# Performance work log

Measured on AMD Instinct MI355X. Metric: run time of the kernel, lower is better.

Reference implementation:

```python
import jax, jax.numpy as jnp
import numpy as np


def setup_inputs() -> dict:
    key = jax.random.key(0)
    kx, kw = jax.random.split(key)
    x = jax.random.normal(kx, (32, 128, 64, 64), dtype=jnp.float32)
    weights = jax.random.normal(kw, (256, 128, 3, 3), dtype=jnp.float32) * 0.05
    return {"x": x, "weights": weights}


def reference(x, weights):
    # Valid-padding, stride-1, no-bias 2D cross-correlation, identical math
    # to the nested-loop HandmadeConv2d (sum over in_ch, kH, kW per output pixel).
    return jax.lax.conv_general_dilated(
        x, weights,
        window_strides=(1, 1),
        padding="VALID",
        dimension_numbers=("NCHW", "OIHW", "NCHW"),
    )
```

## Files before the change

### kernel.cpp

```cpp
#include <hip/hip_runtime.h>
#include <hip/hip_bf16.h>

typedef unsigned short ushort;
typedef unsigned int uint;
typedef __bf16 bf16x8 __attribute__((ext_vector_type(8)));
typedef float f32x4 __attribute__((ext_vector_type(4)));
typedef uint uint4v __attribute__((ext_vector_type(4)));
typedef uint uint2v __attribute__((ext_vector_type(2)));

#define CI 128
#define HIN 64
#define WIN 64
#define CO 256
#define HO 62
#define WO 62
#define NB 32
#define KTOT 1152
#define PIXIMG 3844
#define NPIX 123008
#define XIMG 524288
#define BK 64
#define NKT 18

__device__ __forceinline__ ushort f2bf(float f) {
  uint u = __builtin_bit_cast(uint, f);
  u += 0x7fffu + ((u >> 16) & 1u);
  return (ushort)(u >> 16);
}

__global__ void repack_w_kernel(const float* __restrict__ w, ushort* __restrict__ w2) {
  const int co = blockIdx.x;
  for (int idx = threadIdx.x; idx < KTOT; idx += 256) {
    const int t  = idx >> 7;
    const int ci = idx & 127;
    w2[co * KTOT + idx] = f2bf(w[(co * CI + ci) * 9 + t]);
  }
}

#define XPAD 132
__global__ __launch_bounds__(256) void repack_x_kernel(const float* __restrict__ x,
                                                       ushort* __restrict__ x2) {
  __shared__ float t[WIN * XPAD];
  const int n = blockIdx.y;
  const int h = blockIdx.x;
  const int tid = threadIdx.x;
  const float* src = x + ((size_t)n * CI * HIN + h) * WIN;
  #pragma unroll
  for (int it = 0; it < 8; ++it) {
    const int idx = it * 256 + tid;
    const int ci  = idx >> 4;
    const int w4  = (idx & 15) * 4;
    const float4 v = *reinterpret_cast<const float4*>(src + (size_t)ci * (HIN * WIN) + w4);
    t[(w4 + 0) * XPAD + ci] = v.x;
    t[(w4 + 1) * XPAD + ci] = v.y;
    t[(w4 + 2) * XPAD + ci] = v.z;
    t[(w4 + 3) * XPAD + ci] = v.w;
  }
  __syncthreads();
  ushort* dst = x2 + ((size_t)(n * HIN + h) * WIN) * CI;
  #pragma unroll
  for (int it = 0; it < 4; ++it) {
    const int idx = it * 256 + tid;
    const int w   = idx >> 4;
    const int cig = idx & 15;
    const float* p = &t[w * XPAD + cig * 8];
    uint4v q;
    q[0] = (uint)f2bf(p[0]) | ((uint)f2bf(p[1]) << 16);
    q[1] = (uint)f2bf(p[2]) | ((uint)f2bf(p[3]) << 16);
    q[2] = (uint)f2bf(p[4]) | ((uint)f2bf(p[5]) << 16);
    q[3] = (uint)f2bf(p[6]) | ((uint)f2bf(p[7]) << 16);
    *reinterpret_cast<uint4v*>(dst + (size_t)w * CI + cig * 8) = q;
  }
}

__global__ __launch_bounds__(256, 4)
void conv_nhwc_kernel(const ushort* __restrict__ x2, const ushort* __restrict__ w2,
                      float* __restrict__ out)
{
  __shared__ alignas(16) ushort a_lds[128 * 64];
  __shared__ alignas(16) ushort b_lds[128 * 64];

  const int tid  = threadIdx.x;
  const int lane = tid & 63;
  const int wid  = tid >> 6;
  const int wrow = wid >> 1;
  const int wcol = wid & 1;

  const int nwg = 1922, q8 = nwg >> 3, r8 = nwg & 7;
  const int wg  = blockIdx.x;
  const int xcd = wg & 7, sidx = wg >> 3;
  const int logical = (xcd < r8 ? xcd * (q8 + 1) : r8 * (q8 + 1) + (xcd - r8) * q8) + sidx;
  const int co0 = (logical & 1) * 128;
  const int p0  = (logical >> 1) * 128;

  const int lrow = lane >> 3;
  const int lc   = (lane & 7) ^ lrow;

  const ushort* pB[4];
  #pragma unroll
  for (int i = 0; i < 4; ++i) {
    const int row   = wid * 32 + i * 8 + lrow;
    const int pglob = p0 + row;
    const int nimg  = pglob / PIXIMG;
    const int prem  = pglob - nimg * PIXIMG;
    const int oh    = prem / WO;
    const int ow    = prem - oh * WO;
    pB[i] = x2 + (size_t)((nimg * HIN + oh) * WIN + ow) * CI + lc * 8;
  }
  const ushort* pA = w2 + (size_t)(co0 + wid * 32 + lrow) * KTOT + lc * 8;

  const int frow_a = wrow * 64 + (lane & 15);
  const int frow_b = wcol * 64 + (lane & 15);
  int aoff[2], boff[2];
  #pragma unroll
  for (int kk = 0; kk < 2; ++kk) {
    const int chk = (kk * 4 + (lane >> 4)) ^ (lane & 7);
    aoff[kk] = frow_a * 64 + chk * 8;
    boff[kk] = frow_b * 64 + chk * 8;
  }

  f32x4 acc[4][4];
  #pragma unroll
  for (int i = 0; i < 4; ++i)
    #pragma unroll
    for (int j = 0; j < 4; ++j)
      acc[i][j] = (f32x4){0.f, 0.f, 0.f, 0.f};

  #pragma unroll
  for (int kt = 0; kt < NKT; ++kt) {
    if (kt) __syncthreads();

    const int tap   = kt >> 1;
    const int rr    = (tap * 11) >> 5;
    const int ss    = tap - rr * 3;
    const int coffB = (rr * WIN + ss) * CI + (kt & 1) * 64;
    const int coffA = kt * 64;

    #pragma unroll
    for (int i = 0; i < 4; ++i) {
      const ushort* src = pA + (size_t)i * (8 * KTOT) + coffA;
      __builtin_amdgcn_global_load_lds(
          (const __attribute__((address_space(1))) uint*)(const void*)src,
          (__attribute__((address_space(3))) uint*)(void*)&a_lds[wid * 2048 + i * 512],
          16, 0, 0);
    }
    #pragma unroll
    for (int i = 0; i < 4; ++i) {
      const ushort* src = pB[i] + coffB;
      __builtin_amdgcn_global_load_lds(
          (const __attribute__((address_space(1))) uint*)(const void*)src,
          (__attribute__((address_space(3))) uint*)(void*)&b_lds[wid * 2048 + i * 512],
          16, 0, 0);
    }

    __syncthreads();

    #pragma unroll
    for (int kk = 0; kk < 2; ++kk) {
      bf16x8 af[4], bb[4];
      #pragma unroll
      for (int mi = 0; mi < 4; ++mi)
        af[mi] = *reinterpret_cast<const bf16x8*>(&a_lds[aoff[kk] + mi * (16 * 64)]);
      #pragma unroll
      for (int ni = 0; ni < 4; ++ni)
        bb[ni] = *reinterpret_cast<const bf16x8*>(&b_lds[boff[kk] + ni * (16 * 64)]);
      #pragma unroll
      for (int mi = 0; mi < 4; ++mi)
        #pragma unroll
        for (int ni = 0; ni < 4; ++ni)
          acc[mi][ni] = __builtin_amdgcn_mfma_f32_16x16x32_bf16(af[mi], bb[ni], acc[mi][ni], 0, 0, 0);
    }
  }

  #pragma unroll
  for (int ni = 0; ni < 4; ++ni) {
    const int pix = p0 + wcol * 64 + ni * 16 + (lane & 15);
    const int n2  = pix / PIXIMG;
    const int pr2 = pix - n2 * PIXIMG;
    float* ob = out + (size_t)n2 * (CO * PIXIMG) + pr2
                    + (size_t)(co0 + wrow * 64 + ((lane >> 4) * 4)) * PIXIMG;
    #pragma unroll
    for (int mi = 0; mi < 4; ++mi) {
      float* po = ob + (size_t)mi * (16 * PIXIMG);
      #pragma unroll
      for (int r = 0; r < 4; ++r)
        po[(size_t)r * PIXIMG] = acc[mi][ni][r];
    }
  }
}

__global__ __launch_bounds__(256, 3)
void conv_fallback_kernel(const float* __restrict__ x, const float* __restrict__ wt,
                          float* __restrict__ out)
{
  __shared__ alignas(16) ushort a_lds[128 * 64];
  __shared__ alignas(16) ushort b_lds[128 * 64];

  const int tid  = threadIdx.x;
  const int lane = tid & 63;
  const int wid  = tid >> 6;
  const int wrow = wid >> 1;
  const int wcol = wid & 1;
  const int co0 = blockIdx.x * 128;
  const int p0  = blockIdx.y * 128;

  const int pl    = tid & 127;
  const int kgsel = __builtin_amdgcn_readfirstlane(tid >> 7);
  const int pglob = p0 + pl;
  const int nimg  = pglob / PIXIMG;
  const int prem  = pglob - nimg * PIXIMG;
  const int oh    = prem / WO;
  const int ow    = prem - oh * WO;
  const int xpix  = nimg * XIMG + oh * WIN + ow;

  const int frow_a = wrow * 64 + (lane & 15);
  const int frow_b = wcol * 64 + (lane & 15);
  int aoff[2], boff[2];
  #pragma unroll
  for (int kk = 0; kk < 2; ++kk) {
    const int chk = (kk * 4 + (lane >> 4)) ^ (lane & 7);
    aoff[kk] = frow_a * 64 + chk * 8;
    boff[kk] = frow_b * 64 + chk * 8;
  }

  f32x4 acc[4][4];
  #pragma unroll
  for (int i = 0; i < 4; ++i)
    #pragma unroll
    for (int j = 0; j < 4; ++j)
      acc[i][j] = (f32x4){0.f, 0.f, 0.f, 0.f};

  for (int kt = 0; kt < NKT; ++kt) {
    const int k0 = kt * BK;
    if (kt) __syncthreads();

    #pragma unroll
    for (int it = 0; it < 4; ++it) {
      const int kg = kgsel + it * 2;
      uint pk[4];
      #pragma unroll
      for (int j = 0; j < 8; ++j) {
        const int k  = k0 + kg * 8 + j;
        const int ci = k / 9;
        const int rs = k - ci * 9;
        const int r  = rs / 3;
        const int s  = rs - r * 3;
        const ushort u = f2bf(x[xpix + ci * (HIN * WIN) + r * WIN + s]);
        if (j & 1) pk[j >> 1] |= ((uint)u) << 16;
        else       pk[j >> 1]  = (uint)u;
      }
      uint4v q = {pk[0], pk[1], pk[2], pk[3]};
      *reinterpret_cast<uint4v*>(&b_lds[pl * 64 + ((kg ^ (pl & 7)) * 8)]) = q;
    }

    #pragma unroll
    for (int i = 0; i < 8; ++i) {
      const int id  = i * 256 + tid;
      const int row = id >> 4;
      const int c4  = id & 15;
      const float4 v = *reinterpret_cast<const float4*>(
          wt + (size_t)(co0 + row) * KTOT + k0 + c4 * 4);
      uint2v q;
      q[0] = (uint)f2bf(v.x) | ((uint)f2bf(v.y) << 16);
      q[1] = (uint)f2bf(v.z) | ((uint)f2bf(v.w) << 16);
      *reinterpret_cast<uint2v*>(
          &a_lds[row * 64 + (((c4 >> 1) ^ (row & 7)) * 8) + (c4 & 1) * 4]) = q;
    }

    __syncthreads();

    #pragma unroll
    for (int kk = 0; kk < 2; ++kk) {
      bf16x8 af[4], bb[4];
      #pragma unroll
      for (int mi = 0; mi < 4; ++mi)
        af[mi] = *reinterpret_cast<const bf16x8*>(&a_lds[aoff[kk] + mi * (16 * 64)]);
      #pragma unroll
      for (int ni = 0; ni < 4; ++ni)
        bb[ni] = *reinterpret_cast<const bf16x8*>(&b_lds[boff[kk] + ni * (16 * 64)]);
      #pragma unroll
      for (int mi = 0; mi < 4; ++mi)
        #pragma unroll
        for (int ni = 0; ni < 4; ++ni)
          acc[mi][ni] = __builtin_amdgcn_mfma_f32_16x16x32_bf16(af[mi], bb[ni], acc[mi][ni], 0, 0, 0);
    }
  }

  #pragma unroll
  for (int ni = 0; ni < 4; ++ni) {
    const int pix = p0 + wcol * 64 + ni * 16 + (lane & 15);
    const int n2  = pix / PIXIMG;
    const int pr2 = pix - n2 * PIXIMG;
    float* ob = out + (size_t)n2 * (CO * PIXIMG) + pr2
                    + (size_t)(co0 + wrow * 64 + ((lane >> 4) * 4)) * PIXIMG;
    #pragma unroll
    for (int mi = 0; mi < 4; ++mi) {
      float* po = ob + (size_t)mi * (16 * PIXIMG);
      #pragma unroll
      for (int r = 0; r < 4; ++r)
        po[(size_t)r * PIXIMG] = acc[mi][ni][r];
    }
  }
}

extern "C" void kernel_launch(void* const* d_in, const int* in_sizes, int n_in,
                              void* d_out, int out_size, void* d_ws, size_t ws_size,
                              hipStream_t stream) {
  const float* x  = (const float*)d_in[0];
  const float* wt = (const float*)d_in[1];
  float* out = (float*)d_out;

  ushort* w2 = (ushort*)d_ws;
  ushort* x2 = (ushort*)((char*)d_ws + 589824);

  const size_t need = 589824 + (size_t)NB * XIMG * 2;

  if (ws_size >= need) {
    repack_w_kernel<<<dim3(CO), dim3(256), 0, stream>>>(wt, w2);
    repack_x_kernel<<<dim3(HIN, NB), dim3(256), 0, stream>>>(x, x2);
    conv_nhwc_kernel<<<dim3(1922), dim3(256), 0, stream>>>(x2, w2, out);
  } else {
    conv_fallback_kernel<<<dim3(CO / 128, NPIX / 128), dim3(256), 0, stream>>>(x, wt, out);
  }
}
```

Measured before the change: 104.7 us.

## Replace conv GEMM with 256x256-tile, 8-wave, double-buffered phased pipeline

Replaces the 128x128-tile, 4-wave conv kernel with a 256-pixel by 256-output-channel tile per 512-thread block. It double-buffers 128 KB of LDS and splits each k-step into four MFMA phases that interleave LDS fragment reads, global-to-LDS prefetch of the next k-tiles and barriers, with s_setprio raised around MFMA bursts. The larger tile is meant to halve global reads per FLOP and hide load latency behind compute. In exchange it drops the XCD-aware block remapping, leaves only 481 blocks (under two waves across the CUs), and clamps the out-of-range tail pixels.

Result: slower. 123.4 us (+17.8%).

```diff
diff --git a/kernel.cpp b/kernel.cpp
--- a/kernel.cpp
+++ b/kernel.cpp
@@ -19,7 +19,6 @@
 #define PIXIMG 3844
 #define NPIX 123008
 #define XIMG 524288
-#define BK 64
 #define NKT 18
 
 __device__ __forceinline__ ushort f2bf(float f) {
@@ -73,118 +72,165 @@
   }
 }
 
-__global__ __launch_bounds__(256, 4)
-void conv_nhwc_kernel(const ushort* __restrict__ x2, const ushort* __restrict__ w2,
-                      float* __restrict__ out)
+
+#define GLOAD(SRC, DSTOFF) \
+  __builtin_amdgcn_global_load_lds( \
+      (const __attribute__((address_space(1))) uint*)(const void*)(SRC), \
+      (__attribute__((address_space(3))) uint*)(void*)&lds[DSTOFF], 16, 0, 0)
+
+#define STAGE_A(DB, SLOT, KT) do { \
+  const int _ca = (KT) * 64; \
+  GLOAD(w2 + aOff[(SLOT) >> 1][0] + _ca, (DB) + (SLOT) * 8192 + stgu);       \
+  GLOAD(w2 + aOff[(SLOT) >> 1][1] + _ca, (DB) + (SLOT) * 8192 + stgu + 512); \
+} while (0)
+
+#define STAGE_B(DB, SLOT, KT) do { \
+  const int _tp = (KT) >> 1; \
+  const int _rr = (_tp * 11) >> 5; \
+  const int _cb = (_rr * WIN + (_tp - _rr * 3)) * CI + ((KT) & 1) * 64; \
+  GLOAD(x2 + bOff[(SLOT) >> 1][0] + _cb, (DB) + (SLOT) * 8192 + stgu);       \
+  GLOAD(x2 + bOff[(SLOT) >> 1][1] + _cb, (DB) + (SLOT) * 8192 + stgu + 512); \
+} while (0)
+
+#define PH_LOADS(LDB, ASLOT, BSLOT) do { \
+  _Pragma("unroll") for (int mf = 0; mf < 4; ++mf) { \
+    fa0[mf] = *reinterpret_cast<const bf16x8*>(&lds[(LDB) + (ASLOT) * 8192 + arow + mf * 1024 + ck0]); \
+    fa1[mf] = *reinterpret_cast<const bf16x8*>(&lds[(LDB) + (ASLOT) * 8192 + arow + mf * 1024 + ck1]); } \
+  _Pragma("unroll") for (int nf = 0; nf < 2; ++nf) { \
+    fb0[nf] = *reinterpret_cast<const bf16x8*>(&lds[(LDB) + (BSLOT) * 8192 + brow + nf * 1024 + ck0]); \
+    fb1[nf] = *reinterpret_cast<const bf16x8*>(&lds[(LDB) + (BSLOT) * 8192 + brow + nf * 1024 + ck1]); } \
+} while (0)
+
+#define PH_MMA(MG, NG) do { \
+  __builtin_amdgcn_s_barrier(); \
+  asm volatile("s_waitcnt lgkmcnt(0)" ::: "memory"); \
+  __builtin_amdgcn_s_setprio(1); \
+  _Pragma("unroll") for (int mf = 0; mf < 4; ++mf) \
+    _Pragma("unroll") for (int nf = 0; nf < 2; ++nf) { \
+      acc[(MG) * 4 + mf][(NG) * 2 + nf] = __builtin_amdgcn_mfma_f32_16x16x32_bf16( \
+          fa0[mf], fb0[nf], acc[(MG) * 4 + mf][(NG) * 2 + nf], 0, 0, 0); \
+      acc[(MG) * 4 + mf][(NG) * 2 + nf] = __builtin_amdgcn_mfma_f32_16x16x32_bf16( \
+          fa1[mf], fb1[nf], acc[(MG) * 4 + mf][(NG) * 2 + nf], 0, 0, 0); } \
+  __builtin_amdgcn_s_setprio(0); \
+  __builtin_amdgcn_s_barrier(); \
+} while (0)
+
+__global__ __launch_bounds__(512, 2)
+void conv_8ph_kernel(const ushort* __restrict__ x2, const ushort* __restrict__ w2,
+                     float* __restrict__ out)
 {
-  __shared__ alignas(16) ushort a_lds[128 * 64];
-  __shared__ alignas(16) ushort b_lds[128 * 64];
+  __shared__ alignas(16) ushort lds[65536];
 
   const int tid  = threadIdx.x;
   const int lane = tid & 63;
   const int wid  = tid >> 6;
-  const int wrow = wid >> 1;
-  const int wcol = wid & 1;
-
-  const int nwg = 1922, q8 = nwg >> 3, r8 = nwg & 7;
-  const int wg  = blockIdx.x;
-  const int xcd = wg & 7, sidx = wg >> 3;
-  const int logical = (xcd < r8 ? xcd * (q8 + 1) : r8 * (q8 + 1) + (xcd - r8) * q8) + sidx;
-  const int co0 = (logical & 1) * 128;
-  const int p0  = (logical >> 1) * 128;
+  const int wm   = wid >> 2;
+  const int wn   = wid & 3;
+
+  const int p0 = blockIdx.x * 256;
 
   const int lrow = lane >> 3;
   const int lc   = (lane & 7) ^ lrow;
-
-  const ushort* pB[4];
-  #pragma unroll
-  for (int i = 0; i < 4; ++i) {
-    const int row   = wid * 32 + i * 8 + lrow;
-    const int pglob = p0 + row;
-    const int nimg  = pglob / PIXIMG;
-    const int prem  = pglob - nimg * PIXIMG;
-    const int oh    = prem / WO;
-    const int ow    = prem - oh * WO;
-    pB[i] = x2 + (size_t)((nimg * HIN + oh) * WIN + ow) * CI + lc * 8;
-  }
-  const ushort* pA = w2 + (size_t)(co0 + wid * 32 + lrow) * KTOT + lc * 8;
-
-  const int frow_a = wrow * 64 + (lane & 15);
-  const int frow_b = wcol * 64 + (lane & 15);
-  int aoff[2], boff[2];
-  #pragma unroll
-  for (int kk = 0; kk < 2; ++kk) {
-    const int chk = (kk * 4 + (lane >> 4)) ^ (lane & 7);
-    aoff[kk] = frow_a * 64 + chk * 8;
-    boff[kk] = frow_b * 64 + chk * 8;
-  }
-
-  f32x4 acc[4][4];
-  #pragma unroll
-  for (int i = 0; i < 4; ++i)
+  const int stgu = wid * 1024;
+
+  int aOff[2][2];
+  #pragma unroll
+  for (int h = 0; h < 2; ++h)
+    #pragma unroll
+    for (int j = 0; j < 2; ++j)
+      aOff[h][j] = (h * 128 + wid * 16 + j * 8 + lrow) * KTOT + lc * 8;
+
+  int bOff[2][2];
+  #pragma unroll
+  for (int h = 0; h < 2; ++h)
+    #pragma unroll
+    for (int j = 0; j < 2; ++j) {
+      int pglob = p0 + h * 128 + wid * 16 + j * 8 + lrow;
+      pglob = pglob < NPIX ? pglob : (NPIX - 1);
+      const int nimg = pglob / PIXIMG;
+      const int prem = pglob - nimg * PIXIMG;
+      const int oh   = prem / WO;
+      const int ow   = prem - oh * WO;
+      bOff[h][j] = ((nimg * HIN + oh) * WIN + ow) * CI + lc * 8;
+    }
+
+  const int arow = (wm * 64 + (lane & 15)) * 64;
+  const int brow = (wn * 32 + (lane & 15)) * 64;
+  const int ck0  = ((lane >> 4) ^ (lane & 7)) * 8;
+  const int ck1  = ((4 + (lane >> 4)) ^ (lane & 7)) * 8;
+
+  f32x4 acc[8][4];
+  #pragma unroll
+  for (int i = 0; i < 8; ++i)
     #pragma unroll
     for (int j = 0; j < 4; ++j)
       acc[i][j] = (f32x4){0.f, 0.f, 0.f, 0.f};
 
-  #pragma unroll
-  for (int kt = 0; kt < NKT; ++kt) {
-    if (kt) __syncthreads();
-
-    const int tap   = kt >> 1;
-    const int rr    = (tap * 11) >> 5;
-    const int ss    = tap - rr * 3;
-    const int coffB = (rr * WIN + ss) * CI + (kt & 1) * 64;
-    const int coffA = kt * 64;
-
-    #pragma unroll
-    for (int i = 0; i < 4; ++i) {
-      const ushort* src = pA + (size_t)i * (8 * KTOT) + coffA;
-      __builtin_amdgcn_global_load_lds(
-          (const __attribute__((address_space(1))) uint*)(const void*)src,
-          (__attribute__((address_space(3))) uint*)(void*)&a_lds[wid * 2048 + i * 512],
-          16, 0, 0);
-    }
-    #pragma unroll
-    for (int i = 0; i < 4; ++i) {
-      const ushort* src = pB[i] + coffB;
-      __builtin_amdgcn_global_load_lds(
-          (const __attribute__((address_space(1))) uint*)(const void*)src,
-          (__attribute__((address_space(3))) uint*)(void*)&b_lds[wid * 2048 + i * 512],
-          16, 0, 0);
-    }
-
-    __syncthreads();
-
-    #pragma unroll
-    for (int kk = 0; kk < 2; ++kk) {
-      bf16x8 af[4], bb[4];
-      #pragma unroll
-      for (int mi = 0; mi < 4; ++mi)
-        af[mi] = *reinterpret_cast<const bf16x8*>(&a_lds[aoff[kk] + mi * (16 * 64)]);
-      #pragma unroll
-      for (int ni = 0; ni < 4; ++ni)
-        bb[ni] = *reinterpret_cast<const bf16x8*>(&b_lds[boff[kk] + ni * (16 * 64)]);
-      #pragma unroll
-      for (int mi = 0; mi < 4; ++mi)
+  bf16x8 fa0[4], fa1[4], fb0[2], fb1[2];
+
+  STAGE_B(0, 0, 0);
+  STAGE_A(0, 1, 0);
+  STAGE_B(0, 2, 0);
+  STAGE_A(0, 3, 0);
+  STAGE_B(32768, 0, 1);
+  STAGE_A(32768, 1, 1);
+  asm volatile("s_waitcnt vmcnt(4)" ::: "memory");
+  __builtin_amdgcn_s_barrier();
+
+  int ldb = 0;
+  #pragma unroll 1
+  for (int t = 0; t < 16; ++t) {
+    PH_LOADS(ldb, 1, 0);
+    STAGE_B(ldb ^ 32768, 2, t + 1);
+    STAGE_A(ldb ^ 32768, 3, t + 1);
+    PH_MMA(0, 0);
+    PH_LOADS(ldb, 3, 0);
+    PH_MMA(1, 0);
+    PH_LOADS(ldb, 1, 2);
+    STAGE_B(ldb, 0, t + 2);
+    PH_MMA(0, 1);
+    PH_LOADS(ldb, 3, 2);
+    STAGE_A(ldb, 1, t + 2);
+    asm volatile("s_waitcnt vmcnt(4)" ::: "memory");
+    PH_MMA(1, 1);
+    ldb ^= 32768;
+  }
+  PH_LOADS(ldb, 1, 0);
+  STAGE_B(ldb ^ 32768, 2, 17);
+  STAGE_A(ldb ^ 32768, 3, 17);
+  PH_MMA(0, 0);
+  PH_LOADS(ldb, 3, 0);
+  PH_MMA(1, 0);
+  PH_LOADS(ldb, 1, 2);
+  PH_MMA(0, 1);
+  PH_LOADS(ldb, 3, 2);
+  asm volatile("s_waitcnt vmcnt(0)" ::: "memory");
+  PH_MMA(1, 1);
+  ldb ^= 32768;
+  PH_LOADS(ldb, 1, 0);
+  PH_MMA(0, 0);
+  PH_LOADS(ldb, 3, 0);
+  PH_MMA(1, 0);
+  PH_LOADS(ldb, 1, 2);
+  PH_MMA(0, 1);
+  PH_LOADS(ldb, 3, 2);
+  PH_MMA(1, 1);
+
+  #pragma unroll
+  for (int ni = 0; ni < 4; ++ni) {
+    const int pix = p0 + (ni >> 1) * 128 + wn * 32 + (ni & 1) * 16 + (lane & 15);
+    if (pix < NPIX) {
+      const int n2  = pix / PIXIMG;
+      const int pr2 = pix - n2 * PIXIMG;
+      float* ob = out + (size_t)n2 * (CO * PIXIMG) + pr2;
+      #pragma unroll
+      for (int mi = 0; mi < 8; ++mi) {
+        const int cobase = (mi >> 2) * 128 + wm * 64 + (mi & 3) * 16 + ((lane >> 4) * 4);
+        float* po = ob + (size_t)cobase * PIXIMG;
         #pragma unroll
-        for (int ni = 0; ni < 4; ++ni)
-          acc[mi][ni] = __builtin_amdgcn_mfma_f32_16x16x32_bf16(af[mi], bb[ni], acc[mi][ni], 0, 0, 0);
-    }
-  }
-
-  #pragma unroll
-  for (int ni = 0; ni < 4; ++ni) {
-    const int pix = p0 + wcol * 64 + ni * 16 + (lane & 15);
-    const int n2  = pix / PIXIMG;
-    const int pr2 = pix - n2 * PIXIMG;
-    float* ob = out + (size_t)n2 * (CO * PIXIMG) + pr2
-                    + (size_t)(co0 + wrow * 64 + ((lane >> 4) * 4)) * PIXIMG;
-    #pragma unroll
-    for (int mi = 0; mi < 4; ++mi) {
-      float* po = ob + (size_t)mi * (16 * PIXIMG);
-      #pragma unroll
-      for (int r = 0; r < 4; ++r)
-        po[(size_t)r * PIXIMG] = acc[mi][ni][r];
+        for (int r = 0; r < 4; ++r)
+          po[(size_t)r * PIXIMG] = acc[mi][ni][r];
+      }
     }
   }
 }
@@ -231,7 +277,7 @@
       acc[i][j] = (f32x4){0.f, 0.f, 0.f, 0.f};
 
   for (int kt = 0; kt < NKT; ++kt) {
-    const int k0 = kt * BK;
+    const int k0 = kt * 64;
     if (kt) __syncthreads();
 
     #pragma unroll
@@ -318,7 +364,7 @@
   if (ws_size >= need) {
     repack_w_kernel<<<dim3(CO), dim3(256), 0, stream>>>(wt, w2);
     repack_x_kernel<<<dim3(HIN, NB), dim3(256), 0, stream>>>(x, x2);
-    conv_nhwc_kernel<<<dim3(1922), dim3(256), 0, stream>>>(x2, w2, out);
+    conv_8ph_kernel<<<dim3(481), dim3(512), 0, stream>>>(x2, w2, out);
   } else {
     conv_fallback_kernel<<<dim3(CO / 128, NPIX / 128), dim3(256), 0, stream>>>(x, wt, out);
   }
```
